# Kernel optimization log

Measured on AMD Instinct MI355X. Metric: run time of the kernel, lower is better.

The kernel has to match this reference:

```python
import jax, jax.numpy as jnp
import numpy as np

N_NODES = 50000
NEG_SLOPE = 0.2  # PyG GATConv default leaky_relu slope


def gat_conv(x, edge_src, edge_dst, W, att_src, att_dst, bias, heads, out_ch, concat):
    """PyG-style GATConv. x:[N,Fin], W:[Fin,H*C], att_*:[H,C], bias:[H*C] or [C]."""
    n = x.shape[0]
    h = (x @ W).reshape(n, heads, out_ch)                      # [N,H,C]
    a_src = jnp.einsum('nhc,hc->nh', h, att_src)               # [N,H]
    a_dst = jnp.einsum('nhc,hc->nh', h, att_dst)               # [N,H]
    e = jax.nn.leaky_relu(a_src[edge_src] + a_dst[edge_dst], NEG_SLOPE)  # [E,H]
    # segment softmax over incoming edges of each dst node
    emax = jax.ops.segment_max(e, edge_dst, num_segments=n)    # [N,H]
    p = jnp.exp(e - emax[edge_dst])                            # [E,H]
    denom = jax.ops.segment_sum(p, edge_dst, num_segments=n)   # [N,H]
    coef = p / denom[edge_dst]                                 # [E,H]
    msg = h[edge_src] * coef[:, :, None]                       # [E,H,C]
    out = jax.ops.segment_sum(msg, edge_dst, num_segments=n)   # [N,H,C]
    if concat:
        out = out.reshape(n, heads * out_ch) + bias
    else:
        out = out.mean(axis=1) + bias
    return out


def setup_inputs() -> dict:
    key = jax.random.key(0)
    ks = jax.random.split(key, 10)
    in_ch, n_units, heads, out_ch = 128, 32, 8, 64
    x = jax.random.normal(ks[0], (N_NODES, in_ch), jnp.float32)
    edge_index = jax.random.randint(ks[1], (2, 800000), 0, N_NODES, jnp.int64)
    g = lambda k, shp, fan: jax.random.normal(k, shp, jnp.float32) * (1.0 / np.sqrt(fan))
    return {
        'x': x,
        'edge_index': edge_index,
        'W1': g(ks[2], (in_ch, heads * n_units), in_ch),
        'att_src1': g(ks[3], (heads, n_units), n_units),
        'att_dst1': g(ks[4], (heads, n_units), n_units),
        'b1': jnp.zeros((heads * n_units,), jnp.float32),
        'W2': g(ks[5], (heads * n_units, out_ch), heads * n_units),
        'att_src2': g(ks[6], (1, out_ch), out_ch),
        'att_dst2': g(ks[7], (1, out_ch), out_ch),
        'b2': jnp.zeros((out_ch,), jnp.float32),
    }


def reference(x, edge_index, W1, att_src1, att_dst1, b1, W2, att_src2, att_dst2, b2):
    # add self-loops (PyG GATConv default add_self_loops=True)
    loops = jnp.arange(N_NODES, dtype=edge_index.dtype)
    src = jnp.concatenate([edge_index[0], loops])
    dst = jnp.concatenate([edge_index[1], loops])
    # dropout is identity at inference (training=False)
    h = gat_conv(x, src, dst, W1, att_src1, att_dst1, b1, heads=8, out_ch=32, concat=True)
    h = jax.nn.relu(h)
    out = gat_conv(h, src, dst, W2, att_src2, att_dst2, b2, heads=1, out_ch=64, concat=True)
    return jax.nn.log_softmax(out, axis=1)
```

## Files before the change

### kernel.cpp

```cpp
#include <hip/hip_runtime.h>
#include <hip/hip_bf16.h>
#include <hip/hip_fp8.h>
#include <cmath>


#define HEADS1 8
#define F1 256
#define F2 64
#define NEG_SLOPE 0.2f

typedef unsigned int uint;
typedef unsigned short ushort_t;
typedef unsigned char uchar_t;
typedef __attribute__((ext_vector_type(8))) short bf16x8;
typedef __attribute__((ext_vector_type(4))) float f32x4;
typedef __attribute__((ext_vector_type(2))) float f32x2;

__device__ __forceinline__ float lrelu(float x) {
  return x >= 0.f ? x : NEG_SLOPE * x;
}
__device__ __forceinline__ ushort_t f2bf(float f) {
  uint u = __float_as_uint(f);
  return (ushort_t)((u + 0x7FFFu + ((u >> 16) & 1u)) >> 16);
}
__device__ __forceinline__ float bf2f(ushort_t u) {
  return __uint_as_float(((uint)u) << 16);
}
__device__ __forceinline__ uint pack2(float a, float b) {
  return (uint)f2bf(a) | ((uint)f2bf(b) << 16);
}
__device__ __forceinline__ uchar_t f2fp8(float f) {
  __hip_fp8_e4m3 t(f);
  return (uchar_t)t.__x;
}
__device__ __forceinline__ float fp82f(uchar_t u) {
  __hip_fp8_e4m3 t;
  t.__x = (__hip_fp8_storage_t)u;
  return (float)t;
}
__device__ __forceinline__ f32x4 fp8x4_decode(uint hv) {
#if __has_builtin(__builtin_amdgcn_cvt_pk_f32_fp8)
  f32x2 lo = __builtin_amdgcn_cvt_pk_f32_fp8((int)hv, false);
  f32x2 hi = __builtin_amdgcn_cvt_pk_f32_fp8((int)hv, true);
  return (f32x4){lo.x, lo.y, hi.x, hi.y};
#else
  return (f32x4){fp82f((uchar_t)(hv & 0xff)),
                 fp82f((uchar_t)((hv >> 8) & 0xff)),
                 fp82f((uchar_t)((hv >> 16) & 0xff)),
                 fp82f((uchar_t)(hv >> 24))};
#endif
}

__global__ __launch_bounds__(256) void kernelA(
    const float* __restrict__ W1, const float* __restrict__ W2,
    const float* __restrict__ att_src1, const float* __restrict__ att_dst1,
    const float* __restrict__ att_src2, const float* __restrict__ att_dst2,
    ushort_t* __restrict__ W1ext, ushort_t* __restrict__ W2t,
    float* __restrict__ w_s2, float* __restrict__ w_d2,
    const int* __restrict__ ei, int E0, int Etot, int* __restrict__ counts,
    int* __restrict__ eslot) {
  const int bid = blockIdx.x;
  const int tid = threadIdx.x;
  if (bid < 128) {
    int idx = bid * 256 + tid;
    int r = idx >> 8, c = idx & 255;
    W1ext[(size_t)c * 128 + r] = f2bf(W1[idx]);
  } else if (bid < 192) {
    int idx = (bid - 128) * 256 + tid;
    int r = idx >> 6, c = idx & 63;
    W2t[(size_t)c * 256 + r] = f2bf(W2[idx]);
  } else if (bid < 200) {
    int idx = (bid - 192) * 256 + tid;
    int r16 = idx >> 7;
    int k = idx & 127;
    const float* att = (r16 < 8) ? att_src1 : att_dst1;
    int h = r16 & 7;
    float v = 0.f;
    #pragma unroll
    for (int c = 0; c < 32; ++c)
      v += W1[(size_t)k * 256 + h * 32 + c] * att[h * 32 + c];
    W1ext[(size_t)(256 + r16) * 128 + k] = f2bf(v);
  } else if (bid < 224) {
    int idx = (bid - 200) * 256 + tid;
    W1ext[(size_t)272 * 128 + idx] = 0;
  } else if (bid < 225) {
    int k = tid;
    float as = 0.f, ad = 0.f;
    #pragma unroll
    for (int c = 0; c < 64; ++c) {
      float wv = W2[(size_t)k * 64 + c];
      as += wv * att_src2[c];
      ad += wv * att_dst2[c];
    }
    w_s2[k] = as;
    w_d2[k] = ad;
  } else {
    int e = (bid - 225) * 256 + tid;
    if (e >= Etot) return;
    int d = (e < E0) ? ei[E0 + e] : (e - E0);
    eslot[e] = atomicAdd(&counts[d], 1);
  }
}

__global__ __launch_bounds__(256) void scan_fused(
    const int* __restrict__ counts, int* __restrict__ row_start,
    int* __restrict__ btot, int n) {
  __shared__ int wsum[4];
  __shared__ int s_prev;
  const int tid = threadIdx.x;
  const int lane = tid & 63;
  const int wid = tid >> 6;
  const int base = blockIdx.x * 1024 + tid * 4;
  int c[4], inc[4];
  #pragma unroll
  for (int j = 0; j < 4; ++j)
    c[j] = (base + j < n) ? counts[base + j] : 0;
  inc[0] = c[0];
  #pragma unroll
  for (int j = 1; j < 4; ++j) inc[j] = inc[j - 1] + c[j];
  int tsum = inc[3];
  int wincl = tsum;
  #pragma unroll
  for (int off = 1; off < 64; off <<= 1) {
    int v = __shfl_up(wincl, off, 64);
    if (lane >= off) wincl += v;
  }
  if (lane == 63) wsum[wid] = wincl;
  __syncthreads();
  int woff = 0;
  #pragma unroll
  for (int j = 0; j < 4; ++j)
    if (j < wid) woff += wsum[j];

  if (tid == 255) atomicExch(&btot[blockIdx.x], woff + wincl);

  if (wid == 0) {
    int run = 0;
    if (lane < blockIdx.x) {
      int v;
      do {
        v = atomicAdd(&btot[lane], 0);
      } while (v == 0);
      run = v;
    }
    #pragma unroll
    for (int off = 32; off > 0; off >>= 1) run += __shfl_xor(run, off, 64);
    if (lane == 0) s_prev = run;
  }
  __syncthreads();

  int prefix = s_prev + woff + (wincl - tsum);
  #pragma unroll
  for (int j = 0; j < 4; ++j)
    if (base + j < n) row_start[base + j + 1] = prefix + inc[j];
  if (blockIdx.x == 0 && tid == 0) row_start[0] = 0;
}

__global__ __launch_bounds__(256) void kernelB(
    const float* __restrict__ x, const ushort_t* __restrict__ W1ext,
    uchar_t* __restrict__ h1, int M,
    const int* __restrict__ ei, int E0, int Etot,
    const int* __restrict__ row_start, const int* __restrict__ eslot,
    int* __restrict__ csr_src,
    float* __restrict__ a_src, float* __restrict__ a_dst,
    int GB1) {
  __shared__ char smem[10240];
  const int bid = blockIdx.x;
  const int tid = threadIdx.x;

  if (bid < GB1) {
    ushort_t* As = (ushort_t*)smem;
    ushort_t* Bs = As + 64 * 40;
    const int lane = tid & 63;
    const int wave = tid >> 6;
    const int wr = wave >> 1, wc = wave & 1;
    const int ct = bid % 5;
    const int row0 = (bid / 5) * 64, col0 = ct * 64;
    const int sr = tid >> 2;
    const int sk = (tid & 3) * 8;
    const int l15 = lane & 15;
    const int lk8 = (lane >> 4) * 8;
    const int K = 128;

    f32x4 acc[2][2];
    #pragma unroll
    for (int i = 0; i < 2; ++i)
      #pragma unroll
      for (int j = 0; j < 2; ++j) acc[i][j] = (f32x4){0.f, 0.f, 0.f, 0.f};

    for (int k0 = 0; k0 < K; k0 += 32) {
      const int gr = row0 + sr;
      float4 f0 = {0.f, 0.f, 0.f, 0.f}, f1 = {0.f, 0.f, 0.f, 0.f};
      if (gr < M) {
        f0 = *(const float4*)&x[(size_t)gr * K + k0 + sk];
        f1 = *(const float4*)&x[(size_t)gr * K + k0 + sk + 4];
      }
      uint4 av;
      av.x = pack2(f0.x, f0.y);
      av.y = pack2(f0.z, f0.w);
      av.z = pack2(f1.x, f1.y);
      av.w = pack2(f1.z, f1.w);
      *(uint4*)&As[sr * 40 + sk] = av;
      uint4 bv = *(const uint4*)&W1ext[(size_t)(col0 + sr) * K + k0 + sk];
      *(uint4*)&Bs[sr * 40 + sk] = bv;
      __syncthreads();

      bf16x8 af[2], bfr[2];
      #pragma unroll
      for (int mi = 0; mi < 2; ++mi)
        af[mi] = *(const bf16x8*)&As[(wr * 32 + mi * 16 + l15) * 40 + lk8];
      #pragma unroll
      for (int ni = 0; ni < 2; ++ni)
        bfr[ni] = *(const bf16x8*)&Bs[(wc * 32 + ni * 16 + l15) * 40 + lk8];
      #pragma unroll
      for (int mi = 0; mi < 2; ++mi)
        #pragma unroll
        for (int ni = 0; ni < 2; ++ni)
          acc[mi][ni] = __builtin_amdgcn_mfma_f32_16x16x32_bf16(
              af[mi], bfr[ni], acc[mi][ni], 0, 0, 0);
      __syncthreads();
    }

    #pragma unroll
    for (int mi = 0; mi < 2; ++mi) {
      #pragma unroll
      for (int ni = 0; ni < 2; ++ni) {
        #pragma unroll
        for (int r = 0; r < 4; ++r) {
          int grow = row0 + wr * 32 + mi * 16 + (lane >> 4) * 4 + r;
          int gcol = col0 + wc * 32 + ni * 16 + l15;
          if (grow >= M) continue;
          float v = acc[mi][ni][r];
          if (gcol < 256) {
            h1[(size_t)grow * F1 + gcol] = f2fp8(v);
          } else if (gcol < 264) {
            a_src[(size_t)grow * 8 + (gcol - 256)] = v;
          } else if (gcol < 272) {
            a_dst[(size_t)grow * 8 + (gcol - 264)] = v;
          }
        }
      }
    }
  } else {
    int e = (bid - GB1) * 256 + tid;
    if (e >= Etot) return;
    int s, d;
    if (e < E0) { s = ei[e]; d = ei[E0 + e]; } else { s = d = e - E0; }
    csr_src[row_start[d] + eslot[e]] = s;
  }
}

__global__ __launch_bounds__(256) void gemm_bf16(
    const ushort_t* __restrict__ Ab, const ushort_t* __restrict__ Bt,
    ushort_t* __restrict__ Cb, int M, int N, int K) {
  __shared__ ushort_t As[64 * 40];
  __shared__ ushort_t Bs[64 * 40];
  const int tid = threadIdx.x;
  const int lane = tid & 63;
  const int wave = tid >> 6;
  const int wr = wave >> 1, wc = wave & 1;
  const int row0 = blockIdx.y * 64, col0 = blockIdx.x * 64;
  const int sr = tid >> 2;
  const int sk = (tid & 3) * 8;
  const int l15 = lane & 15;
  const int lk8 = (lane >> 4) * 8;

  f32x4 acc[2][2];
  #pragma unroll
  for (int i = 0; i < 2; ++i)
    #pragma unroll
    for (int j = 0; j < 2; ++j) acc[i][j] = (f32x4){0.f, 0.f, 0.f, 0.f};

  for (int k0 = 0; k0 < K; k0 += 32) {
    const int gr = row0 + sr;
    uint4 av = {0u, 0u, 0u, 0u};
    if (gr < M) av = *(const uint4*)&Ab[(size_t)gr * K + k0 + sk];
    *(uint4*)&As[sr * 40 + sk] = av;
    uint4 bv = *(const uint4*)&Bt[(size_t)(col0 + sr) * K + k0 + sk];
    *(uint4*)&Bs[sr * 40 + sk] = bv;
    __syncthreads();

    bf16x8 af[2], bfr[2];
    #pragma unroll
    for (int mi = 0; mi < 2; ++mi)
      af[mi] = *(const bf16x8*)&As[(wr * 32 + mi * 16 + l15) * 40 + lk8];
    #pragma unroll
    for (int ni = 0; ni < 2; ++ni)
      bfr[ni] = *(const bf16x8*)&Bs[(wc * 32 + ni * 16 + l15) * 40 + lk8];
    #pragma unroll
    for (int mi = 0; mi < 2; ++mi)
      #pragma unroll
      for (int ni = 0; ni < 2; ++ni)
        acc[mi][ni] = __builtin_amdgcn_mfma_f32_16x16x32_bf16(
            af[mi], bfr[ni], acc[mi][ni], 0, 0, 0);
    __syncthreads();
  }

  #pragma unroll
  for (int mi = 0; mi < 2; ++mi) {
    #pragma unroll
    for (int ni = 0; ni < 2; ++ni) {
      #pragma unroll
      for (int r = 0; r < 4; ++r) {
        int grow = row0 + wr * 32 + mi * 16 + (lane >> 4) * 4 + r;
        int gcol = col0 + wc * 32 + ni * 16 + l15;
        if (grow < M) Cb[(size_t)grow * N + gcol] = f2bf(acc[mi][ni][r]);
      }
    }
  }
}

__global__ __launch_bounds__(256) void gather1(
    const int* __restrict__ csr_src, const int* __restrict__ row_start,
    const float* __restrict__ a_src, const float* __restrict__ a_dst,
    const uchar_t* __restrict__ h1, const float* __restrict__ b,
    const float* __restrict__ ws2, const float* __restrict__ wd2,
    ushort_t* __restrict__ out, float* __restrict__ a_src2,
    float* __restrict__ a_dst2, int n) {
  const int d = blockIdx.x * 4 + (threadIdx.x >> 6);
  const int lane = threadIdx.x & 63;
  if (d >= n) return;
  const int rs = row_start[d];
  const int deg = row_start[d + 1] - rs;
  const int pe = lane >> 3;
  const int ph = lane & 7;
  const int hsel = lane >> 3;
  const float adv = a_dst[d * 8 + ph];

  float dpart = 0.f;
  f32x4 acc = {0.f, 0.f, 0.f, 0.f};

  for (int t0 = 0; t0 < deg; t0 += 8) {
    const int myi = t0 + pe;
    int mys = 0;
    float myc = 0.f;
    if (myi < deg) {
      mys = csr_src[rs + myi];
      myc = __expf(lrelu(a_src[mys * 8 + ph] + adv));
      dpart += myc;
    }
    #pragma unroll
    for (int jj = 0; jj < 8; ++jj) {
      float cf = __shfl(myc, jj * 8 + hsel, 64);
      int s = __shfl(mys, jj * 8, 64);
      uint hv = *(const uint*)&h1[(size_t)s * F1 + lane * 4];
      f32x4 hd = fp8x4_decode(hv);
      acc[0] += cf * hd[0];
      acc[1] += cf * hd[1];
      acc[2] += cf * hd[2];
      acc[3] += cf * hd[3];
    }
  }

  dpart += __shfl_xor(dpart, 8, 64);
  dpart += __shfl_xor(dpart, 16, 64);
  dpart += __shfl_xor(dpart, 32, 64);
  const float rden = 1.f / __shfl(dpart, hsel, 64);

  const int ch = lane * 4;
  ushort4 ob;
  float ps = 0.f, pd = 0.f;
  #pragma unroll
  for (int j = 0; j < 4; ++j) {
    float v = fmaxf(acc[j] * rden + b[ch + j], 0.f);
    ushort_t bv = f2bf(v);
    ((ushort_t*)&ob)[j] = bv;
    float r = bf2f(bv);
    ps += r * ws2[ch + j];
    pd += r * wd2[ch + j];
  }
  *(ushort4*)&out[(size_t)d * F1 + ch] = ob;
  #pragma unroll
  for (int off = 32; off > 0; off >>= 1) {
    ps += __shfl_xor(ps, off, 64);
    pd += __shfl_xor(pd, off, 64);
  }
  if (lane == 0) {
    a_src2[d] = ps;
    a_dst2[d] = pd;
  }
}

__global__ __launch_bounds__(256) void gather2(
    const int* __restrict__ csr_src, const int* __restrict__ row_start,
    const float* __restrict__ a_src, const float* __restrict__ a_dst,
    const ushort_t* __restrict__ h2, const float* __restrict__ b,
    float* __restrict__ out, int n) {
  const int d = blockIdx.x * 4 + (threadIdx.x >> 6);
  const int lane = threadIdx.x & 63;
  if (d >= n) return;
  const int rs = row_start[d];
  const int deg = row_start[d + 1] - rs;
  const float adv = a_dst[d];

  const int sub = lane >> 4;
  const int q = lane & 15;
  float lsum = 0.f;
  f32x4 acc = {0.f, 0.f, 0.f, 0.f};
  for (int t0 = 0; t0 < deg; t0 += 64) {
    int myi = t0 + lane;
    int mys = 0;
    float myc = 0.f;
    if (myi < deg) {
      mys = csr_src[rs + myi];
      myc = __expf(lrelu(a_src[mys] + adv));
      lsum += myc;
    }
    const int nt = min(64, deg - t0);
    const int ntp = (nt + 3) & ~3;
    for (int e = sub; e < ntp; e += 4) {
      float cf = __shfl(myc, e, 64);
      int s = __shfl(mys, e, 64);
      ushort4 hv = *(const ushort4*)&h2[(size_t)s * F2 + q * 4];
      acc[0] += cf * bf2f(hv.x);
      acc[1] += cf * bf2f(hv.y);
      acc[2] += cf * bf2f(hv.z);
      acc[3] += cf * bf2f(hv.w);
    }
  }
  #pragma unroll
  for (int off = 32; off > 0; off >>= 1) lsum += __shfl_xor(lsum, off, 64);
  const float rden = 1.f / lsum;

  #pragma unroll
  for (int j = 0; j < 4; ++j) {
    acc[j] += __shfl_xor(acc[j], 16, 64);
    acc[j] += __shfl_xor(acc[j], 32, 64);
  }
  float vx = __shfl(acc[0], lane >> 2, 64);
  float vy = __shfl(acc[1], lane >> 2, 64);
  float vz = __shfl(acc[2], lane >> 2, 64);
  float vw = __shfl(acc[3], lane >> 2, 64);
  int c3 = lane & 3;
  float v = (c3 == 0) ? vx : (c3 == 1) ? vy : (c3 == 2) ? vz : vw;
  v = v * rden + b[lane];
  float m = v;
  #pragma unroll
  for (int off = 32; off > 0; off >>= 1) m = fmaxf(m, __shfl_xor(m, off, 64));
  float ex = __expf(v - m);
  float ss = ex;
  #pragma unroll
  for (int off = 32; off > 0; off >>= 1) ss += __shfl_xor(ss, off, 64);
  out[(size_t)d * F2 + lane] = v - m - __logf(ss);
}

extern "C" void kernel_launch(void* const* d_in, const int* in_sizes, int n_in,
                              void* d_out, int out_size, void* d_ws,
                              size_t ws_size, hipStream_t stream) {
  const float* x        = (const float*)d_in[0];
  const int*   ei       = (const int*)d_in[1];
  const float* W1       = (const float*)d_in[2];
  const float* att_src1 = (const float*)d_in[3];
  const float* att_dst1 = (const float*)d_in[4];
  const float* b1       = (const float*)d_in[5];
  const float* W2       = (const float*)d_in[6];
  const float* att_src2 = (const float*)d_in[7];
  const float* att_dst2 = (const float*)d_in[8];
  const float* b2       = (const float*)d_in[9];

  const int N = in_sizes[0] / 128;
  const int E0 = in_sizes[1] / 2;
  const int Etot = E0 + N;
  const int nb1024 = (N + 1023) / 1024;

  char* w = (char*)d_ws;
  size_t off = 0;
  auto alloc = [&](size_t bytes) {
    char* p = w + off;
    off += (bytes + 255) & ~(size_t)255;
    return p;
  };
  uchar_t*  h1        = (uchar_t*) alloc((size_t)N * F1 * 1);
  ushort_t* h1out     = (ushort_t*)alloc((size_t)N * F1 * 2);
  ushort_t* h2b       = (ushort_t*)alloc((size_t)N * F2 * 2);
  int*      csr_src   = (int*)     alloc((size_t)Etot * 4);
  int*      eslot     = (int*)     alloc((size_t)Etot * 4);
  int*      row_start = (int*)     alloc((size_t)(N + 1) * 4);
  int*      cc        = (int*)     alloc(((size_t)N + nb1024) * 4);
  int*      counts    = cc;
  int*      btot      = cc + N;
  float*    a_src1    = (float*)   alloc((size_t)N * HEADS1 * 4);
  float*    a_dst1    = (float*)   alloc((size_t)N * HEADS1 * 4);
  float*    a_src2    = (float*)   alloc((size_t)N * 4);
  float*    a_dst2    = (float*)   alloc((size_t)N * 4);
  ushort_t* W1ext     = (ushort_t*)alloc(320 * 128 * 2);
  ushort_t* W2t       = (ushort_t*)alloc(256 * 64 * 2);
  float*    w_s2      = (float*)   alloc(256 * 4);
  float*    w_d2      = (float*)   alloc(256 * 4);

  hipMemsetAsync(cc, 0, ((size_t)N + nb1024) * 4, stream);

  dim3 blk(256);
  const int eb = (Etot + 255) / 256;
  const int gy = (N + 63) / 64;
  const int GB1 = 5 * gy;

  kernelA<<<225 + eb, blk, 0, stream>>>(W1, W2, att_src1, att_dst1, att_src2,
                                        att_dst2, W1ext, W2t, w_s2, w_d2,
                                        ei, E0, Etot, counts, eslot);
  scan_fused<<<nb1024, blk, 0, stream>>>(counts, row_start, btot, N);

  kernelB<<<GB1 + eb, blk, 0, stream>>>(
      x, W1ext, h1, N, ei, E0, Etot, row_start, eslot, csr_src,
      a_src1, a_dst1, GB1);

  gather1<<<(N + 3) / 4, blk, 0, stream>>>(csr_src, row_start, a_src1, a_dst1,
                                           h1, b1, w_s2, w_d2, h1out, a_src2,
                                           a_dst2, N);

  gemm_bf16<<<dim3(F2 / 64, gy), blk, 0, stream>>>(h1out, W2t, h2b, N, F2, F1);
  gather2<<<(N + 3) / 4, blk, 0, stream>>>(csr_src, row_start, a_src2, a_dst2,
                                           h2b, b2, (float*)d_out, N);
}
```

Measured before the change: 169.9 us.

## Compute all column tiles per row block in kernelB and stage fp8 h1 in LDS

The first-layer GEMM now gives each block a full 64-row slab. The x tile is converted to bf16 once into LDS with full K, then the block loops over the five column tiles instead of spreading them across five blocks. The fp8 results are collected in a shared row buffer and written out as 16-byte vector stores instead of scattered single-byte stores. The cost is a much larger LDS footprint per block (about 52 KB) and five times fewer GEMM blocks, which may reduce occupancy and parallelism.

```diff
diff --git a/kernel.cpp b/kernel.cpp
--- a/kernel.cpp
+++ b/kernel.cpp
@@ -8,6 +8,8 @@
 #define F1 256
 #define F2 64
 #define NEG_SLOPE 0.2f
+#define KP 136
+#define HP 272
 
 typedef unsigned int uint;
 typedef unsigned short ushort_t;
@@ -164,30 +166,24 @@
     int* __restrict__ csr_src,
     float* __restrict__ a_src, float* __restrict__ a_dst,
     int GB1) {
-  __shared__ char smem[10240];
+  __shared__ ushort_t AsF[64 * KP];
+  __shared__ ushort_t BsF[64 * KP];
+  __shared__ uchar_t  h1row[64 * HP];
   const int bid = blockIdx.x;
   const int tid = threadIdx.x;
 
   if (bid < GB1) {
-    ushort_t* As = (ushort_t*)smem;
-    ushort_t* Bs = As + 64 * 40;
     const int lane = tid & 63;
     const int wave = tid >> 6;
     const int wr = wave >> 1, wc = wave & 1;
-    const int ct = bid % 5;
-    const int row0 = (bid / 5) * 64, col0 = ct * 64;
+    const int row0 = bid * 64;
     const int sr = tid >> 2;
     const int sk = (tid & 3) * 8;
     const int l15 = lane & 15;
     const int lk8 = (lane >> 4) * 8;
     const int K = 128;
 
-    f32x4 acc[2][2];
-    #pragma unroll
-    for (int i = 0; i < 2; ++i)
-      #pragma unroll
-      for (int j = 0; j < 2; ++j) acc[i][j] = (f32x4){0.f, 0.f, 0.f, 0.f};
-
+    #pragma unroll
     for (int k0 = 0; k0 < K; k0 += 32) {
       const int gr = row0 + sr;
       float4 f0 = {0.f, 0.f, 0.f, 0.f}, f1 = {0.f, 0.f, 0.f, 0.f};
@@ -200,45 +196,78 @@
       av.y = pack2(f0.z, f0.w);
       av.z = pack2(f1.x, f1.y);
       av.w = pack2(f1.z, f1.w);
-      *(uint4*)&As[sr * 40 + sk] = av;
-      uint4 bv = *(const uint4*)&W1ext[(size_t)(col0 + sr) * K + k0 + sk];
-      *(uint4*)&Bs[sr * 40 + sk] = bv;
+      *(uint4*)&AsF[sr * KP + k0 + sk] = av;
+    }
+
+    for (int ct = 0; ct < 5; ++ct) {
+      const int col0 = ct * 64;
       __syncthreads();
-
-      bf16x8 af[2], bfr[2];
       #pragma unroll
-      for (int mi = 0; mi < 2; ++mi)
-        af[mi] = *(const bf16x8*)&As[(wr * 32 + mi * 16 + l15) * 40 + lk8];
+      for (int k0 = 0; k0 < K; k0 += 32) {
+        uint4 bv = *(const uint4*)&W1ext[(size_t)(col0 + sr) * K + k0 + sk];
+        *(uint4*)&BsF[sr * KP + k0 + sk] = bv;
+      }
+      __syncthreads();
+
+      f32x4 acc[2][2];
       #pragma unroll
-      for (int ni = 0; ni < 2; ++ni)
-        bfr[ni] = *(const bf16x8*)&Bs[(wc * 32 + ni * 16 + l15) * 40 + lk8];
+      for (int i = 0; i < 2; ++i)
+        #pragma unroll
+        for (int j = 0; j < 2; ++j) acc[i][j] = (f32x4){0.f, 0.f, 0.f, 0.f};
+
       #pragma unroll
-      for (int mi = 0; mi < 2; ++mi)
+      for (int k0 = 0; k0 < K; k0 += 32) {
+        bf16x8 af[2], bfr[2];
+        #pragma unroll
+        for (int mi = 0; mi < 2; ++mi)
+          af[mi] = *(const bf16x8*)&AsF[(wr * 32 + mi * 16 + l15) * KP + k0 + lk8];
         #pragma unroll
         for (int ni = 0; ni < 2; ++ni)
-          acc[mi][ni] = __builtin_amdgcn_mfma_f32_16x16x32_bf16(
-              af[mi], bfr[ni], acc[mi][ni], 0, 0, 0);
-      __syncthreads();
-    }
-
-    #pragma unroll
-    for (int mi = 0; mi < 2; ++mi) {
+          bfr[ni] = *(const bf16x8*)&BsF[(wc * 32 + ni * 16 + l15) * KP + k0 + lk8];
+        #pragma unroll
+        for (int mi = 0; mi < 2; ++mi)
+          #pragma unroll
+          for (int ni = 0; ni < 2; ++ni)
+            acc[mi][ni] = __builtin_amdgcn_mfma_f32_16x16x32_bf16(
+                af[mi], bfr[ni], acc[mi][ni], 0, 0, 0);
+      }
+
+      if (ct < 4) {
+        #pragma unroll
+        for (int mi = 0; mi < 2; ++mi)
+          #pragma unroll
+          for (int ni = 0; ni < 2; ++ni)
+            #pragma unroll
+            for (int r = 0; r < 4; ++r) {
+              int lrow = wr * 32 + mi * 16 + (lane >> 4) * 4 + r;
+              int lcol = col0 + wc * 32 + ni * 16 + l15;
+              h1row[lrow * HP + lcol] = f2fp8(acc[mi][ni][r]);
+            }
+      } else {
+        #pragma unroll
+        for (int mi = 0; mi < 2; ++mi)
+          #pragma unroll
+          for (int ni = 0; ni < 2; ++ni)
+            #pragma unroll
+            for (int r = 0; r < 4; ++r) {
+              int grow = row0 + wr * 32 + mi * 16 + (lane >> 4) * 4 + r;
+              int c = wc * 32 + ni * 16 + l15;
+              if (grow >= M) continue;
+              float v = acc[mi][ni][r];
+              if (c < 8) a_src[(size_t)grow * 8 + c] = v;
+              else if (c < 16) a_dst[(size_t)grow * 8 + (c - 8)] = v;
+            }
+      }
+    }
+
+    __syncthreads();
+    const int r = tid >> 2, q = tid & 3;
+    const int grow = row0 + r;
+    if (grow < M) {
       #pragma unroll
-      for (int ni = 0; ni < 2; ++ni) {
-        #pragma unroll
-        for (int r = 0; r < 4; ++r) {
-          int grow = row0 + wr * 32 + mi * 16 + (lane >> 4) * 4 + r;
-          int gcol = col0 + wc * 32 + ni * 16 + l15;
-          if (grow >= M) continue;
-          float v = acc[mi][ni][r];
-          if (gcol < 256) {
-            h1[(size_t)grow * F1 + gcol] = f2fp8(v);
-          } else if (gcol < 264) {
-            a_src[(size_t)grow * 8 + (gcol - 256)] = v;
-          } else if (gcol < 272) {
-            a_dst[(size_t)grow * 8 + (gcol - 264)] = v;
-          }
-        }
+      for (int j = 0; j < 4; ++j) {
+        uint4 v = *(uint4*)&h1row[r * HP + q * 64 + j * 16];
+        *(uint4*)&h1[(size_t)grow * F1 + q * 64 + j * 16] = v;
       }
     }
   } else {
@@ -493,7 +522,7 @@
   dim3 blk(256);
   const int eb = (Etot + 255) / 256;
   const int gy = (N + 63) / 64;
-  const int GB1 = 5 * gy;
+  const int GB1 = gy;
 
   kernelA<<<225 + eb, blk, 0, stream>>>(W1, W2, att_src1, att_dst1, att_src2,
                                         att_dst2, W1ext, W2t, w_s2, w_d2,
```

After: 164.7 us. 3.0% less time.
